# Kernel optimization log

Measured on AMD Instinct MI355X. Metric: run time of the kernel, lower is better.

The kernel has to match this reference:

```python
import jax, jax.numpy as jnp
import numpy as np

T, B, D_IN, H = 512, 128, 512, 1024
TAU, DT = 10.0, 1.0
CONST = DT / TAU  # dt/tau leaky-integration constant


def setup_inputs() -> dict:
    key = jax.random.key(0)
    k1, k2, k3, k4, k5 = jax.random.split(key, 5)
    s_in = 1.0 / np.sqrt(D_IN)
    s_h = 1.0 / np.sqrt(H)
    return {
        "x": jax.random.normal(k1, (T, B, D_IN), dtype=jnp.float32),
        "hidden": jnp.zeros((B, H), dtype=jnp.float32),
        "W_in": jax.random.uniform(k2, (H, D_IN), jnp.float32, -s_in, s_in),
        "b_in": jax.random.uniform(k3, (H,), jnp.float32, -s_in, s_in),
        "W_h": jax.random.uniform(k4, (H, H), jnp.float32, -s_h, s_h),
        "b_h": jax.random.uniform(k5, (H,), jnp.float32, -s_h, s_h),
    }


def reference(x, hidden, W_in, b_in, W_h, b_h):
    # Faithful to the source: `hidden` is never updated inside the torch loop,
    # so every step uses the SAME initial hidden. This makes all T steps
    # independent and fully vectorizable:
    #   out[t] = hidden*(1-c) + c*relu(x[t] @ W_in^T + b_in + hidden @ W_h^T + b_h)
    h_term = hidden @ W_h.T + b_h                     # [B, H], computed once
    pre = jnp.einsum('tbd,hd->tbh', x, W_in) + b_in   # [T, B, H]
    out = hidden[None] * (1.0 - CONST) + CONST * jax.nn.relu(pre + h_term[None])
    return (out, hidden)
```

## Files before the change

kernel.cpp:

```cpp
#include <hip/hip_runtime.h>
#include <stdint.h>

#define T_DIM 512
#define B_DIM 128
#define DIN   512
#define H_DIM 1024
#define M_DIM (T_DIM * B_DIM)
#define OUT_ELEMS 67108864

typedef __attribute__((ext_vector_type(8))) short bf16x8;
typedef __attribute__((ext_vector_type(4))) float f32x4;
typedef unsigned short u16;

static __device__ __forceinline__ u16 f2bf(float f) {
    union { float f; uint32_t u; } v; v.f = f;
    uint32_t u = v.u;
    uint32_t r = (u + 0x7FFFu + ((u >> 16) & 1u)) >> 16;
    return (u16)r;
}

typedef const __attribute__((address_space(1))) void GASV;
typedef __attribute__((address_space(3))) void LASV;
static __device__ __forceinline__ void gload_lds16(const void* g, void* l) {
    __builtin_amdgcn_global_load_lds((GASV*)g, (LASV*)l, 16, 0, 0);
}

__global__ __launch_bounds__(256) void k_convert(
    const float* __restrict__ x, const float* __restrict__ W_in,
    const float* __restrict__ W_h, const float* __restrict__ hidden,
    u16* __restrict__ x_bf, u16* __restrict__ Win_bf,
    u16* __restrict__ Wh_bf, u16* __restrict__ hid_bf,
    float* __restrict__ out_hidden)
{
    int u = blockIdx.x * 256 + threadIdx.x;
    const float* src; u16* dst; int i;
    if (u < 4194304)      { i = u;           src = x;      dst = x_bf;   }
    else if (u < 4259840) { i = u - 4194304; src = W_in;   dst = Win_bf; }
    else if (u < 4390912) { i = u - 4259840; src = W_h;    dst = Wh_bf;  }
    else                  { i = u - 4390912; src = hidden; dst = hid_bf; }
    float4 v0 = reinterpret_cast<const float4*>(src)[2 * (size_t)i];
    float4 v1 = reinterpret_cast<const float4*>(src)[2 * (size_t)i + 1];
    union { bf16x8 v; u16 s[8]; } r;
    r.s[0] = f2bf(v0.x); r.s[1] = f2bf(v0.y);
    r.s[2] = f2bf(v0.z); r.s[3] = f2bf(v0.w);
    r.s[4] = f2bf(v1.x); r.s[5] = f2bf(v1.y);
    r.s[6] = f2bf(v1.z); r.s[7] = f2bf(v1.w);
    reinterpret_cast<bf16x8*>(dst)[i] = r.v;
    if (u >= 4390912) {
        reinterpret_cast<float4*>(out_hidden)[2 * i]     = v0;
        reinterpret_cast<float4*>(out_hidden)[2 * i + 1] = v1;
    }
}

__global__ __launch_bounds__(256, 2) void k_bias2(
    const u16* __restrict__ hid_bf, const u16* __restrict__ Wh_bf,
    const float* __restrict__ b_in, const float* __restrict__ b_h,
    float* __restrict__ bias2)
{
    __shared__ alignas(16) char lds[16384];
    const int tid = threadIdx.x;
    const int mt = blockIdx.x & 1, nt = blockIdx.x >> 1;
    const int m0 = mt * 64, n0 = nt * 64;
    const int l = tid & 63, w = tid >> 6;
    const int wm = w >> 1, wn = w & 1;
    const int r = l & 15, q = l >> 4;

    f32x4 acc[2][2] = {};

    for (int kb = 0; kb < 1024; kb += 64) {
        __syncthreads();
        #pragma unroll
        for (int i = 0; i < 2; ++i) {
            int idx = tid + i * 256;
            int row = idx >> 3, koff = (idx & 7) * 8;
            int off = (row * 128 + koff * 2) ^ ((row & 7) << 4);
            bf16x8 av = *reinterpret_cast<const bf16x8*>(&hid_bf[(m0 + row) * 1024 + kb + koff]);
            *reinterpret_cast<bf16x8*>(&lds[off]) = av;
            bf16x8 bv = *reinterpret_cast<const bf16x8*>(&Wh_bf[(n0 + row) * 1024 + kb + koff]);
            *reinterpret_cast<bf16x8*>(&lds[8192 + off]) = bv;
        }
        __syncthreads();
        #pragma unroll
        for (int kk = 0; kk < 2; ++kk) {
            bf16x8 a[2], b[2];
            #pragma unroll
            for (int mi = 0; mi < 2; ++mi) {
                int row = wm * 32 + mi * 16 + r;
                int off = (row * 128 + kk * 64 + q * 16) ^ ((row & 7) << 4);
                a[mi] = *reinterpret_cast<const bf16x8*>(&lds[off]);
            }
            #pragma unroll
            for (int ni = 0; ni < 2; ++ni) {
                int row = wn * 32 + ni * 16 + r;
                int off = 8192 + ((row * 128 + kk * 64 + q * 16) ^ ((row & 7) << 4));
                b[ni] = *reinterpret_cast<const bf16x8*>(&lds[off]);
            }
            #pragma unroll
            for (int mi = 0; mi < 2; ++mi)
                #pragma unroll
                for (int ni = 0; ni < 2; ++ni)
                    acc[mi][ni] = __builtin_amdgcn_mfma_f32_16x16x32_bf16(
                        a[mi], b[ni], acc[mi][ni], 0, 0, 0);
        }
    }
    #pragma unroll
    for (int mi = 0; mi < 2; ++mi)
        #pragma unroll
        for (int ni = 0; ni < 2; ++ni)
            #pragma unroll
            for (int reg = 0; reg < 4; ++reg) {
                int brow = m0 + wm * 32 + mi * 16 + q * 4 + reg;
                int col  = n0 + wn * 32 + ni * 16 + r;
                bias2[brow * 1024 + col] = acc[mi][ni][reg] + b_in[col] + b_h[col];
            }
}

__global__ __launch_bounds__(256, 4) void k_main(
    const u16* __restrict__ x_bf,
    const u16* __restrict__ Win_bf,
    const float* __restrict__ bias2,
    const float* __restrict__ hidden,
    float* __restrict__ out)
{
    __shared__ alignas(16) char ldsA[16384];
    __shared__ alignas(16) char ldsB[16384];

    const int tid = threadIdx.x;
    const int bid = (int)blockIdx.x;
    const int wgid = (bid & 7) * 512 + (bid >> 3);
    const int nt = wgid & 7, mt = wgid >> 3;
    const int m0 = mt * 128, n0 = nt * 128;
    const int l = tid & 63, w = tid >> 6;
    const int wm = w >> 1, wn = w & 1;
    const int r = l & 15, q = l >> 4;

    const int rs = l >> 3;
    const int ck = (l & 7) ^ rs;

    f32x4 acc[4][4] = {};

    for (int k = 0; k < 8; ++k) {
        #pragma unroll
        for (int j = 0; j < 4; ++j) {
            const int seg = w * 4 + j;
            const int row = seg * 8 + rs;
            gload_lds16(&x_bf[(size_t)(m0 + row) * 512 + k * 64 + ck * 8],
                        &ldsA[seg * 1024]);
            gload_lds16(&Win_bf[(size_t)(n0 + row) * 512 + k * 64 + ck * 8],
                        &ldsB[seg * 1024]);
        }
        __syncthreads();

        #pragma unroll
        for (int kk = 0; kk < 2; ++kk) {
            bf16x8 a[4], b[4];
            #pragma unroll
            for (int mi = 0; mi < 4; ++mi) {
                int row = wm * 64 + mi * 16 + r;
                int off = (row * 128 + kk * 64 + q * 16) ^ ((row & 7) << 4);
                a[mi] = *reinterpret_cast<const bf16x8*>(&ldsA[off]);
            }
            #pragma unroll
            for (int ni = 0; ni < 4; ++ni) {
                int row = wn * 64 + ni * 16 + r;
                int off = (row * 128 + kk * 64 + q * 16) ^ ((row & 7) << 4);
                b[ni] = *reinterpret_cast<const bf16x8*>(&ldsB[off]);
            }
            #pragma unroll
            for (int mi = 0; mi < 4; ++mi)
                #pragma unroll
                for (int ni = 0; ni < 4; ++ni)
                    acc[mi][ni] = __builtin_amdgcn_mfma_f32_16x16x32_bf16(
                        b[ni], a[mi], acc[mi][ni], 0, 0, 0);
        }
        __syncthreads();
    }

    #pragma unroll
    for (int mi = 0; mi < 4; ++mi) {
        const int m = m0 + wm * 64 + mi * 16 + r;
        const int b = m & 127;
        #pragma unroll
        for (int ni = 0; ni < 4; ++ni) {
            const int n = n0 + wn * 64 + ni * 16 + q * 4;
            float4 bb = *reinterpret_cast<const float4*>(&bias2[b * 1024 + n]);
            float4 hh = *reinterpret_cast<const float4*>(&hidden[b * 1024 + n]);
            f32x4 v = acc[mi][ni];
            float4 o;
            o.x = 0.9f * hh.x + 0.1f * fmaxf(v[0] + bb.x, 0.0f);
            o.y = 0.9f * hh.y + 0.1f * fmaxf(v[1] + bb.y, 0.0f);
            o.z = 0.9f * hh.z + 0.1f * fmaxf(v[2] + bb.z, 0.0f);
            o.w = 0.9f * hh.w + 0.1f * fmaxf(v[3] + bb.w, 0.0f);
            *reinterpret_cast<float4*>(&out[(size_t)m * 1024 + n]) = o;
        }
    }
}

extern "C" void kernel_launch(void* const* d_in, const int* in_sizes, int n_in,
                              void* d_out, int out_size, void* d_ws, size_t ws_size,
                              hipStream_t stream) {
    const float* x      = (const float*)d_in[0];
    const float* hidden = (const float*)d_in[1];
    const float* W_in   = (const float*)d_in[2];
    const float* b_in   = (const float*)d_in[3];
    const float* W_h    = (const float*)d_in[4];
    const float* b_h    = (const float*)d_in[5];
    float* out = (float*)d_out;

    char* ws = (char*)d_ws;
    u16*   x_bf   = (u16*)  (ws + 0);
    u16*   Win_bf = (u16*)  (ws + 67108864);
    u16*   Wh_bf  = (u16*)  (ws + 68157440);
    u16*   hid_bf = (u16*)  (ws + 70254592);
    float* bias2  = (float*)(ws + 70516736);

    float* out_hidden = out + OUT_ELEMS;

    k_convert<<<17216, 256, 0, stream>>>(x, W_in, W_h, hidden,
                                         x_bf, Win_bf, Wh_bf, hid_bf, out_hidden);
    k_bias2<<<32, 256, 0, stream>>>(hid_bf, Wh_bf, b_in, b_h, bias2);
    k_main<<<4096, 256, 0, stream>>>(x_bf, Win_bf, bias2, hidden, out);
}
```

Measured before the change: 208.8 us.

## Enlarge main GEMM tile to 256x256 with double-buffered LDS prefetch

The main GEMM block grows from 128x128 tiles with 256 threads to 256x256 tiles with 512 threads. LDS is double-buffered so the next K slice loads directly into LDS while the current one is being multiplied. The compute is split into four phases fenced by explicit barriers, waitcnts, sched_barriers and setprio to interleave LDS reads with MFMA. This cuts global traffic per FLOP and hides load latency, but uses 128KB of LDS per block, many more accumulator registers and many more barriers. The workload is likely dominated by the 256MB output write, so gains may be limited.

```diff
diff --git a/kernel.cpp b/kernel.cpp
--- a/kernel.cpp
+++ b/kernel.cpp
@@ -24,6 +24,11 @@
 static __device__ __forceinline__ void gload_lds16(const void* g, void* l) {
     __builtin_amdgcn_global_load_lds((GASV*)g, (LASV*)l, 16, 0, 0);
 }
+
+#define SB0()   __builtin_amdgcn_sched_barrier(0)
+#define BAR()   do { __builtin_amdgcn_s_barrier(); SB0(); } while (0)
+#define LGKM0() do { asm volatile("s_waitcnt lgkmcnt(0)" ::: "memory"); SB0(); } while (0)
+#define VM0()   do { asm volatile("s_waitcnt vmcnt(0)" ::: "memory"); SB0(); } while (0)
 
 __global__ __launch_bounds__(256) void k_convert(
     const float* __restrict__ x, const float* __restrict__ W_in,
@@ -115,76 +120,150 @@
             }
 }
 
-__global__ __launch_bounds__(256, 4) void k_main(
+__global__ __launch_bounds__(512, 2) void k_main(
     const u16* __restrict__ x_bf,
     const u16* __restrict__ Win_bf,
     const float* __restrict__ bias2,
     const float* __restrict__ hidden,
     float* __restrict__ out)
 {
-    __shared__ alignas(16) char ldsA[16384];
-    __shared__ alignas(16) char ldsB[16384];
+    __shared__ alignas(16) char ldsA[2][32768];
+    __shared__ alignas(16) char ldsB[2][32768];
 
     const int tid = threadIdx.x;
     const int bid = (int)blockIdx.x;
-    const int wgid = (bid & 7) * 512 + (bid >> 3);
-    const int nt = wgid & 7, mt = wgid >> 3;
-    const int m0 = mt * 128, n0 = nt * 128;
+    const int wgid = (bid & 7) * 128 + (bid >> 3);
+    const int nt = wgid & 3, mt = wgid >> 2;
+    const int m0 = mt * 256, n0 = nt * 256;
+
     const int l = tid & 63, w = tid >> 6;
-    const int wm = w >> 1, wn = w & 1;
-    const int r = l & 15, q = l >> 4;
-
-    const int rs = l >> 3;
-    const int ck = (l & 7) ^ rs;
-
-    f32x4 acc[4][4] = {};
-
-    for (int k = 0; k < 8; ++k) {
-        #pragma unroll
-        for (int j = 0; j < 4; ++j) {
-            const int seg = w * 4 + j;
-            const int row = seg * 8 + rs;
-            gload_lds16(&x_bf[(size_t)(m0 + row) * 512 + k * 64 + ck * 8],
-                        &ldsA[seg * 1024]);
-            gload_lds16(&Win_bf[(size_t)(n0 + row) * 512 + k * 64 + ck * 8],
-                        &ldsB[seg * 1024]);
+    const int wm = w >> 2, wn = w & 3;
+    const int r = l & 15, q = (l >> 4) & 3;
+    const int swz = (r & 7) << 4;
+
+    const int rbase = tid >> 3;
+    const int cs = (tid & 7) ^ (rbase & 7);
+    const int soff = cs * 8;
+
+    const int aBase = (wm * 128 + r) * 128 + q * 16;
+    const int bBase = (wn * 64 + r) * 128 + q * 16;
+
+    f32x4 acc[8][4] = {};
+
+    #pragma unroll
+    for (int i = 0; i < 4; ++i) {
+        const int row = rbase + i * 64;
+        gload_lds16(&x_bf[(size_t)(m0 + row) * 512 + soff],
+                    &ldsA[0][(tid + i * 512) * 16]);
+        gload_lds16(&Win_bf[(size_t)(n0 + row) * 512 + soff],
+                    &ldsB[0][(tid + i * 512) * 16]);
+    }
+    VM0();
+    BAR();
+
+    #pragma unroll 2
+    for (int kt = 0; kt < 8; ++kt) {
+        const int cur = kt & 1;
+        const char* bufA = &ldsA[cur][0];
+        const char* bufB = &ldsB[cur][0];
+        bf16x8 a[4], b[4];
+
+        #pragma unroll
+        for (int mi = 0; mi < 4; ++mi)
+            a[mi] = *reinterpret_cast<const bf16x8*>(bufA + ((aBase + mi * 2048) ^ swz));
+        #pragma unroll
+        for (int ni = 0; ni < 4; ++ni)
+            b[ni] = *reinterpret_cast<const bf16x8*>(bufB + ((bBase + ni * 2048) ^ swz));
+        if (kt < 7) {
+            const int nxt = cur ^ 1;
+            #pragma unroll
+            for (int i = 0; i < 4; ++i) {
+                const int row = rbase + i * 64;
+                gload_lds16(&x_bf[(size_t)(m0 + row) * 512 + (kt + 1) * 64 + soff],
+                            &ldsA[nxt][(tid + i * 512) * 16]);
+                gload_lds16(&Win_bf[(size_t)(n0 + row) * 512 + (kt + 1) * 64 + soff],
+                            &ldsB[nxt][(tid + i * 512) * 16]);
+            }
         }
-        __syncthreads();
-
-        #pragma unroll
-        for (int kk = 0; kk < 2; ++kk) {
-            bf16x8 a[4], b[4];
-            #pragma unroll
-            for (int mi = 0; mi < 4; ++mi) {
-                int row = wm * 64 + mi * 16 + r;
-                int off = (row * 128 + kk * 64 + q * 16) ^ ((row & 7) << 4);
-                a[mi] = *reinterpret_cast<const bf16x8*>(&ldsA[off]);
-            }
-            #pragma unroll
-            for (int ni = 0; ni < 4; ++ni) {
-                int row = wn * 64 + ni * 16 + r;
-                int off = (row * 128 + kk * 64 + q * 16) ^ ((row & 7) << 4);
-                b[ni] = *reinterpret_cast<const bf16x8*>(&ldsB[off]);
-            }
-            #pragma unroll
-            for (int mi = 0; mi < 4; ++mi)
-                #pragma unroll
-                for (int ni = 0; ni < 4; ++ni)
-                    acc[mi][ni] = __builtin_amdgcn_mfma_f32_16x16x32_bf16(
-                        b[ni], a[mi], acc[mi][ni], 0, 0, 0);
-        }
-        __syncthreads();
+        SB0();
+        BAR();
+        LGKM0();
+        __builtin_amdgcn_s_setprio(1);
+        #pragma unroll
+        for (int mi = 0; mi < 4; ++mi)
+            #pragma unroll
+            for (int ni = 0; ni < 4; ++ni)
+                acc[mi][ni] = __builtin_amdgcn_mfma_f32_16x16x32_bf16(
+                    b[ni], a[mi], acc[mi][ni], 0, 0, 0);
+        __builtin_amdgcn_s_setprio(0);
+        SB0();
+        BAR();
+
+        #pragma unroll
+        for (int mi = 0; mi < 4; ++mi)
+            a[mi] = *reinterpret_cast<const bf16x8*>(bufA + ((aBase + (mi + 4) * 2048) ^ swz));
+        SB0();
+        BAR();
+        LGKM0();
+        __builtin_amdgcn_s_setprio(1);
+        #pragma unroll
+        for (int mi = 0; mi < 4; ++mi)
+            #pragma unroll
+            for (int ni = 0; ni < 4; ++ni)
+                acc[mi + 4][ni] = __builtin_amdgcn_mfma_f32_16x16x32_bf16(
+                    b[ni], a[mi], acc[mi + 4][ni], 0, 0, 0);
+        __builtin_amdgcn_s_setprio(0);
+        SB0();
+        BAR();
+
+        #pragma unroll
+        for (int mi = 0; mi < 4; ++mi)
+            a[mi] = *reinterpret_cast<const bf16x8*>(bufA + ((aBase + mi * 2048 + 64) ^ swz));
+        #pragma unroll
+        for (int ni = 0; ni < 4; ++ni)
+            b[ni] = *reinterpret_cast<const bf16x8*>(bufB + ((bBase + ni * 2048 + 64) ^ swz));
+        SB0();
+        BAR();
+        LGKM0();
+        __builtin_amdgcn_s_setprio(1);
+        #pragma unroll
+        for (int mi = 0; mi < 4; ++mi)
+            #pragma unroll
+            for (int ni = 0; ni < 4; ++ni)
+                acc[mi][ni] = __builtin_amdgcn_mfma_f32_16x16x32_bf16(
+                    b[ni], a[mi], acc[mi][ni], 0, 0, 0);
+        __builtin_amdgcn_s_setprio(0);
+        SB0();
+        BAR();
+
+        #pragma unroll
+        for (int mi = 0; mi < 4; ++mi)
+            a[mi] = *reinterpret_cast<const bf16x8*>(bufA + ((aBase + (mi + 4) * 2048 + 64) ^ swz));
+        SB0();
+        BAR();
+        LGKM0();
+        __builtin_amdgcn_s_setprio(1);
+        #pragma unroll
+        for (int mi = 0; mi < 4; ++mi)
+            #pragma unroll
+            for (int ni = 0; ni < 4; ++ni)
+                acc[mi + 4][ni] = __builtin_amdgcn_mfma_f32_16x16x32_bf16(
+                    b[ni], a[mi], acc[mi + 4][ni], 0, 0, 0);
+        __builtin_amdgcn_s_setprio(0);
+        SB0();
+        VM0();
+        BAR();
     }
 
     #pragma unroll
-    for (int mi = 0; mi < 4; ++mi) {
-        const int m = m0 + wm * 64 + mi * 16 + r;
-        const int b = m & 127;
+    for (int mi = 0; mi < 8; ++mi) {
+        const int m = m0 + wm * 128 + mi * 16 + r;
+        const int bb_ = m & 127;
         #pragma unroll
         for (int ni = 0; ni < 4; ++ni) {
             const int n = n0 + wn * 64 + ni * 16 + q * 4;
-            float4 bb = *reinterpret_cast<const float4*>(&bias2[b * 1024 + n]);
-            float4 hh = *reinterpret_cast<const float4*>(&hidden[b * 1024 + n]);
+            float4 bb = *reinterpret_cast<const float4*>(&bias2[bb_ * 1024 + n]);
+            float4 hh = *reinterpret_cast<const float4*>(&hidden[bb_ * 1024 + n]);
             f32x4 v = acc[mi][ni];
             float4 o;
             o.x = 0.9f * hh.x + 0.1f * fmaxf(v[0] + bb.x, 0.0f);
@@ -219,5 +298,5 @@
     k_convert<<<17216, 256, 0, stream>>>(x, W_in, W_h, hidden,
                                          x_bf, Win_bf, Wh_bf, hid_bf, out_hidden);
     k_bias2<<<32, 256, 0, stream>>>(hid_bf, Wh_bf, b_in, b_h, bias2);
-    k_main<<<4096, 256, 0, stream>>>(x_bf, Win_bf, bias2, hidden, out);
-}
+    k_main<<<1024, 512, 0, stream>>>(x_bf, Win_bf, bias2, hidden, out);
+}
```

New measurement: 300.1 us. 1.44x slower.

## Double-buffer LDS tiles in main GEMM to overlap loads with MFMA

Applied to the files above, without the earlier changes.

The main GEMM kernel now uses two LDS buffers for the A and B tiles. It prefetches the next K-slice with global_load_lds while the MFMAs consume the current one, which removes the trailing barrier in each iteration. The goal is to hide global-to-LDS latency behind compute. In exchange, LDS per block doubles to 64KB and the occupancy hint drops from 4 to 2 blocks per CU, so there is less latency hiding through wave parallelism.

```diff
diff --git a/kernel.cpp b/kernel.cpp
--- a/kernel.cpp
+++ b/kernel.cpp
@@ -115,15 +115,15 @@
             }
 }
 
-__global__ __launch_bounds__(256, 4) void k_main(
+__global__ __launch_bounds__(256, 2) void k_main(
     const u16* __restrict__ x_bf,
     const u16* __restrict__ Win_bf,
     const float* __restrict__ bias2,
     const float* __restrict__ hidden,
     float* __restrict__ out)
 {
-    __shared__ alignas(16) char ldsA[16384];
-    __shared__ alignas(16) char ldsB[16384];
+    __shared__ alignas(16) char ldsA[2][16384];
+    __shared__ alignas(16) char ldsB[2][16384];
 
     const int tid = threadIdx.x;
     const int bid = (int)blockIdx.x;
@@ -139,17 +139,33 @@
 
     f32x4 acc[4][4] = {};
 
+    #pragma unroll
+    for (int j = 0; j < 4; ++j) {
+        const int seg = w * 4 + j;
+        const int row = seg * 8 + rs;
+        gload_lds16(&x_bf[(size_t)(m0 + row) * 512 + ck * 8],
+                    &ldsA[0][seg * 1024]);
+        gload_lds16(&Win_bf[(size_t)(n0 + row) * 512 + ck * 8],
+                    &ldsB[0][seg * 1024]);
+    }
+
+    #pragma unroll
     for (int k = 0; k < 8; ++k) {
-        #pragma unroll
-        for (int j = 0; j < 4; ++j) {
-            const int seg = w * 4 + j;
-            const int row = seg * 8 + rs;
-            gload_lds16(&x_bf[(size_t)(m0 + row) * 512 + k * 64 + ck * 8],
-                        &ldsA[seg * 1024]);
-            gload_lds16(&Win_bf[(size_t)(n0 + row) * 512 + k * 64 + ck * 8],
-                        &ldsB[seg * 1024]);
-        }
+        const int cur = k & 1;
         __syncthreads();
+
+        if (k < 7) {
+            const int nxt = cur ^ 1;
+            #pragma unroll
+            for (int j = 0; j < 4; ++j) {
+                const int seg = w * 4 + j;
+                const int row = seg * 8 + rs;
+                gload_lds16(&x_bf[(size_t)(m0 + row) * 512 + (k + 1) * 64 + ck * 8],
+                            &ldsA[nxt][seg * 1024]);
+                gload_lds16(&Win_bf[(size_t)(n0 + row) * 512 + (k + 1) * 64 + ck * 8],
+                            &ldsB[nxt][seg * 1024]);
+            }
+        }
 
         #pragma unroll
         for (int kk = 0; kk < 2; ++kk) {
@@ -158,13 +174,13 @@
             for (int mi = 0; mi < 4; ++mi) {
                 int row = wm * 64 + mi * 16 + r;
                 int off = (row * 128 + kk * 64 + q * 16) ^ ((row & 7) << 4);
-                a[mi] = *reinterpret_cast<const bf16x8*>(&ldsA[off]);
+                a[mi] = *reinterpret_cast<const bf16x8*>(&ldsA[cur][off]);
             }
             #pragma unroll
             for (int ni = 0; ni < 4; ++ni) {
                 int row = wn * 64 + ni * 16 + r;
                 int off = (row * 128 + kk * 64 + q * 16) ^ ((row & 7) << 4);
-                b[ni] = *reinterpret_cast<const bf16x8*>(&ldsB[off]);
+                b[ni] = *reinterpret_cast<const bf16x8*>(&ldsB[cur][off]);
             }
             #pragma unroll
             for (int mi = 0; mi < 4; ++mi)
@@ -173,7 +189,6 @@
                     acc[mi][ni] = __builtin_amdgcn_mfma_f32_16x16x32_bf16(
                         b[ni], a[mi], acc[mi][ni], 0, 0, 0);
         }
-        __syncthreads();
     }
 
     #pragma unroll
```

Result: slower. 219.8 us (+5.3%).

## Fuse x fp32-to-bf16 conversion into GEMM and load operands directly to registers

Applied to the files above, without the earlier changes.

Drops the separate pass that converted all of x to bf16 in a workspace. The main GEMM now reads fp32 x directly, converts it in registers, and loads MFMA fragments straight from global memory with register double-buffering instead of staging through LDS. This removes a full extra read and write of x, but there is no LDS reuse, so each wave fetches its own A and B fragments and the tiles are re-read across waves. Occupancy is also lowered to 2 blocks per CU.

```diff
diff --git a/kernel.cpp b/kernel.cpp
--- a/kernel.cpp
+++ b/kernel.cpp
@@ -1,4 +1,5 @@
 #include <hip/hip_runtime.h>
+#include <hip/hip_bf16.h>
 #include <stdint.h>
 
 #define T_DIM 512
@@ -19,25 +20,26 @@
     return (u16)r;
 }
 
-typedef const __attribute__((address_space(1))) void GASV;
-typedef __attribute__((address_space(3))) void LASV;
-static __device__ __forceinline__ void gload_lds16(const void* g, void* l) {
-    __builtin_amdgcn_global_load_lds((GASV*)g, (LASV*)l, 16, 0, 0);
-}
-
-__global__ __launch_bounds__(256) void k_convert(
-    const float* __restrict__ x, const float* __restrict__ W_in,
-    const float* __restrict__ W_h, const float* __restrict__ hidden,
-    u16* __restrict__ x_bf, u16* __restrict__ Win_bf,
-    u16* __restrict__ Wh_bf, u16* __restrict__ hid_bf,
+static __device__ __forceinline__ bf16x8 cvt8(float4 lo, float4 hi) {
+    union { bf16x8 v; __hip_bfloat16 h[8]; } u;
+    u.h[0] = __float2bfloat16(lo.x); u.h[1] = __float2bfloat16(lo.y);
+    u.h[2] = __float2bfloat16(lo.z); u.h[3] = __float2bfloat16(lo.w);
+    u.h[4] = __float2bfloat16(hi.x); u.h[5] = __float2bfloat16(hi.y);
+    u.h[6] = __float2bfloat16(hi.z); u.h[7] = __float2bfloat16(hi.w);
+    return u.v;
+}
+
+__global__ __launch_bounds__(256) void k_prep(
+    const float* __restrict__ W_in, const float* __restrict__ W_h,
+    const float* __restrict__ hidden,
+    u16* __restrict__ Win_bf, u16* __restrict__ Wh_bf, u16* __restrict__ hid_bf,
     float* __restrict__ out_hidden)
 {
     int u = blockIdx.x * 256 + threadIdx.x;
     const float* src; u16* dst; int i;
-    if (u < 4194304)      { i = u;           src = x;      dst = x_bf;   }
-    else if (u < 4259840) { i = u - 4194304; src = W_in;   dst = Win_bf; }
-    else if (u < 4390912) { i = u - 4259840; src = W_h;    dst = Wh_bf;  }
-    else                  { i = u - 4390912; src = hidden; dst = hid_bf; }
+    if (u < 65536)       { i = u;          src = W_in;   dst = Win_bf; }
+    else if (u < 196608) { i = u - 65536;  src = W_h;    dst = Wh_bf;  }
+    else                 { i = u - 196608; src = hidden; dst = hid_bf; }
     float4 v0 = reinterpret_cast<const float4*>(src)[2 * (size_t)i];
     float4 v1 = reinterpret_cast<const float4*>(src)[2 * (size_t)i + 1];
     union { bf16x8 v; u16 s[8]; } r;
@@ -46,7 +48,7 @@
     r.s[4] = f2bf(v1.x); r.s[5] = f2bf(v1.y);
     r.s[6] = f2bf(v1.z); r.s[7] = f2bf(v1.w);
     reinterpret_cast<bf16x8*>(dst)[i] = r.v;
-    if (u >= 4390912) {
+    if (u >= 196608) {
         reinterpret_cast<float4*>(out_hidden)[2 * i]     = v0;
         reinterpret_cast<float4*>(out_hidden)[2 * i + 1] = v1;
     }
@@ -115,16 +117,13 @@
             }
 }
 
-__global__ __launch_bounds__(256, 4) void k_main(
-    const u16* __restrict__ x_bf,
-    const u16* __restrict__ Win_bf,
+__global__ __launch_bounds__(256, 2) void k_main(
+    const float* __restrict__ x,
+    const u16*   __restrict__ Win_bf,
     const float* __restrict__ bias2,
     const float* __restrict__ hidden,
     float* __restrict__ out)
 {
-    __shared__ alignas(16) char ldsA[16384];
-    __shared__ alignas(16) char ldsB[16384];
-
     const int tid = threadIdx.x;
     const int bid = (int)blockIdx.x;
     const int wgid = (bid & 7) * 512 + (bid >> 3);
@@ -134,46 +133,50 @@
     const int wm = w >> 1, wn = w & 1;
     const int r = l & 15, q = l >> 4;
 
-    const int rs = l >> 3;
-    const int ck = (l & 7) ^ rs;
+    const float* aptr = x      + (size_t)(m0 + wm * 64 + r) * 512 + q * 8;
+    const u16*   bptr = Win_bf + (size_t)(n0 + wn * 64 + r) * 512 + q * 8;
 
     f32x4 acc[4][4] = {};
 
-    for (int k = 0; k < 8; ++k) {
-        #pragma unroll
-        for (int j = 0; j < 4; ++j) {
-            const int seg = w * 4 + j;
-            const int row = seg * 8 + rs;
-            gload_lds16(&x_bf[(size_t)(m0 + row) * 512 + k * 64 + ck * 8],
-                        &ldsA[seg * 1024]);
-            gload_lds16(&Win_bf[(size_t)(n0 + row) * 512 + k * 64 + ck * 8],
-                        &ldsB[seg * 1024]);
-        }
-        __syncthreads();
-
-        #pragma unroll
-        for (int kk = 0; kk < 2; ++kk) {
-            bf16x8 a[4], b[4];
+    bf16x8 acur[4], bcur[4], bnxt[4];
+    float4 af0[4], af1[4];
+
+    #pragma unroll
+    for (int mi = 0; mi < 4; ++mi) {
+        const float* s = aptr + (size_t)mi * 8192;
+        af0[mi] = *reinterpret_cast<const float4*>(s);
+        af1[mi] = *reinterpret_cast<const float4*>(s + 4);
+        bcur[mi] = *reinterpret_cast<const bf16x8*>(bptr + (size_t)mi * 8192);
+    }
+    #pragma unroll
+    for (int mi = 0; mi < 4; ++mi)
+        acur[mi] = cvt8(af0[mi], af1[mi]);
+
+    #pragma unroll
+    for (int kk = 0; kk < 16; ++kk) {
+        if (kk < 15) {
             #pragma unroll
             for (int mi = 0; mi < 4; ++mi) {
-                int row = wm * 64 + mi * 16 + r;
-                int off = (row * 128 + kk * 64 + q * 16) ^ ((row & 7) << 4);
-                a[mi] = *reinterpret_cast<const bf16x8*>(&ldsA[off]);
-            }
-            #pragma unroll
-            for (int ni = 0; ni < 4; ++ni) {
-                int row = wn * 64 + ni * 16 + r;
-                int off = (row * 128 + kk * 64 + q * 16) ^ ((row & 7) << 4);
-                b[ni] = *reinterpret_cast<const bf16x8*>(&ldsB[off]);
-            }
-            #pragma unroll
-            for (int mi = 0; mi < 4; ++mi)
-                #pragma unroll
-                for (int ni = 0; ni < 4; ++ni)
-                    acc[mi][ni] = __builtin_amdgcn_mfma_f32_16x16x32_bf16(
-                        b[ni], a[mi], acc[mi][ni], 0, 0, 0);
-        }
-        __syncthreads();
+                const float* s = aptr + (size_t)mi * 8192 + (kk + 1) * 32;
+                af0[mi] = *reinterpret_cast<const float4*>(s);
+                af1[mi] = *reinterpret_cast<const float4*>(s + 4);
+                bnxt[mi] = *reinterpret_cast<const bf16x8*>(
+                    bptr + (size_t)mi * 8192 + (kk + 1) * 32);
+            }
+        }
+        #pragma unroll
+        for (int mi = 0; mi < 4; ++mi)
+            #pragma unroll
+            for (int ni = 0; ni < 4; ++ni)
+                acc[mi][ni] = __builtin_amdgcn_mfma_f32_16x16x32_bf16(
+                    bcur[ni], acur[mi], acc[mi][ni], 0, 0, 0);
+        if (kk < 15) {
+            #pragma unroll
+            for (int mi = 0; mi < 4; ++mi) {
+                acur[mi] = cvt8(af0[mi], af1[mi]);
+                bcur[mi] = bnxt[mi];
+            }
+        }
     }
 
     #pragma unroll
@@ -208,16 +211,15 @@
     float* out = (float*)d_out;
 
     char* ws = (char*)d_ws;
-    u16*   x_bf   = (u16*)  (ws + 0);
-    u16*   Win_bf = (u16*)  (ws + 67108864);
-    u16*   Wh_bf  = (u16*)  (ws + 68157440);
-    u16*   hid_bf = (u16*)  (ws + 70254592);
-    float* bias2  = (float*)(ws + 70516736);
+    u16*   Win_bf = (u16*)  (ws + 0);
+    u16*   Wh_bf  = (u16*)  (ws + 1048576);
+    u16*   hid_bf = (u16*)  (ws + 3145728);
+    float* bias2  = (float*)(ws + 3407872);
 
     float* out_hidden = out + OUT_ELEMS;
 
-    k_convert<<<17216, 256, 0, stream>>>(x, W_in, W_h, hidden,
-                                         x_bf, Win_bf, Wh_bf, hid_bf, out_hidden);
+    k_prep<<<832, 256, 0, stream>>>(W_in, W_h, hidden,
+                                    Win_bf, Wh_bf, hid_bf, out_hidden);
     k_bias2<<<32, 256, 0, stream>>>(hid_bf, Wh_bf, b_in, b_h, bias2);
-    k_main<<<4096, 256, 0, stream>>>(x_bf, Win_bf, bias2, hidden, out);
-}
+    k_main<<<4096, 256, 0, stream>>>(x, Win_bf, bias2, hidden, out);
+}
```

Measured after the change: 473.4 us. 127% more time.
